# Kernel tuning notes

Hardware: AMD Instinct MI355X
Metric: run time of the kernel (lower is better)

The kernel has to match this reference:

```python
import jax, jax.numpy as jnp
import numpy as np

EXP = 2          # self.exp
NEG = -1e9       # mask fill value
B, N1, DIM, F = 4, 1024, 1024, 4
N = N1 + 1
NTOT = F * N     # 4100


def _normalize(x):
    # L2-normalize along last dim; also return the norm (keepdims)
    n = jnp.sqrt(jnp.sum(x * x, axis=-1, keepdims=True))
    return x / n, n


def setup_inputs() -> dict:
    key = jax.random.key(0)
    k1, k2 = jax.random.split(key)
    lhs = jax.random.normal(k1, (B, N1, DIM), dtype=jnp.float32)
    rhs = jax.random.normal(k2, (B, NTOT, DIM), dtype=jnp.float32)
    return {"lhs": lhs, "rhs": rhs}


def reference(lhs, rhs):
    b, n1, dim = lhs.shape
    n = n1 + 1
    ntot = rhs.shape[1]
    f = ntot // n

    lhs_n, lhs_norm = _normalize(lhs)          # (B,N1,D), (B,N1,1)
    rhs_n, _ = _normalize(rhs)                 # (B,Ntot,D)

    # cosine similarity GEMM + power epilogue
    sim = jnp.einsum('bnd,bmd->bnm', lhs_n, rhs_n) ** EXP   # (B,N1,Ntot)

    # view as (B, N1, F, N); torch masks:
    #   sim4[..., -N1:][~eye] = -1e9   (off-diagonal of last N1 cols)
    #   sim4[..., 0] = -1e9            (first col of each frame)
    # net keep condition: j == i + 1
    sim4 = sim.reshape(b, n1, f, n)
    i = jnp.arange(n1)[:, None, None]   # (N1,1,1)
    j = jnp.arange(n)[None, None, :]    # (1,1,N)
    keep = (j == i + 1)                 # (N1,1,N), broadcasts over F
    sim4 = jnp.where(keep, sim4, jnp.float32(NEG))

    return sim4.reshape(b, n1, ntot), lhs_norm
```

## Files before the change

### kernel.cpp

```cpp
#include <hip/hip_runtime.h>

#define BB   4
#define N1   1024
#define DIM  1024
#define FF   4
#define NN   1025
#define NTOT (FF * NN)
#define SIM_TOTAL ((size_t)BB * N1 * NTOT)
#define NEGV (-1e9f)

__device__ __forceinline__ float wave_reduce_sum(float v) {
#pragma unroll
    for (int off = 32; off > 0; off >>= 1)
        v += __shfl_down(v, off, 64);
    return v;
}

__global__ __launch_bounds__(256)
void lcs_kernel(const float* __restrict__ lhs,
                const float* __restrict__ rhs,
                float* __restrict__ out) {
    const int row = blockIdx.x;
    const int b   = row >> 10;
    const int i   = row & (N1 - 1);
    const int tid = threadIdx.x;

    const float4* lrow = (const float4*)(lhs + (size_t)row * DIM);
    const float4 lv = lrow[tid];
    float p_l2 = lv.x * lv.x + lv.y * lv.y + lv.z * lv.z + lv.w * lv.w;

    float p_dot[FF], p_r2[FF];
#pragma unroll
    for (int f = 0; f < FF; ++f) {
        const size_t rrow_idx = (size_t)b * NTOT + (size_t)f * NN + (i + 1);
        const float4* rrow = (const float4*)(rhs + rrow_idx * DIM);
        const float4 rv = rrow[tid];
        p_dot[f] = lv.x * rv.x + lv.y * rv.y + lv.z * rv.z + lv.w * rv.w;
        p_r2[f]  = rv.x * rv.x + rv.y * rv.y + rv.z * rv.z + rv.w * rv.w;
    }

    float4* orow4 = (float4*)(out + (size_t)row * NTOT);
    const float4 negv = make_float4(NEGV, NEGV, NEGV, NEGV);
#pragma unroll
    for (int k = tid; k < NTOT / 4; k += 256)
        orow4[k] = negv;

    float vals[9];
    vals[0] = p_l2;
#pragma unroll
    for (int f = 0; f < FF; ++f) {
        vals[1 + 2 * f] = p_dot[f];
        vals[2 + 2 * f] = p_r2[f];
    }

    __shared__ float red[4][9];
    const int wave = tid >> 6;
    const int lane = tid & 63;
#pragma unroll
    for (int q = 0; q < 9; ++q) {
        const float r = wave_reduce_sum(vals[q]);
        if (lane == 0) red[wave][q] = r;
    }
    __syncthreads();

    if (tid == 0) {
        float s[9];
#pragma unroll
        for (int q = 0; q < 9; ++q)
            s[q] = red[0][q] + red[1][q] + red[2][q] + red[3][q];

        const float l2 = s[0];
        float* orow = out + (size_t)row * NTOT;
#pragma unroll
        for (int f = 0; f < FF; ++f) {
            const float dot = s[1 + 2 * f];
            const float r2  = s[2 + 2 * f];
            orow[f * NN + i + 1] = (dot * dot) / (l2 * r2);
        }
        out[SIM_TOTAL + row] = sqrtf(l2);
    }
}

extern "C" void kernel_launch(void* const* d_in, const int* in_sizes, int n_in,
                              void* d_out, int out_size, void* d_ws, size_t ws_size,
                              hipStream_t stream) {
    const float* lhs = (const float*)d_in[0];
    const float* rhs = (const float*)d_in[1];
    float* out = (float*)d_out;

    lcs_kernel<<<BB * N1, 256, 0, stream>>>(lhs, rhs, out);
}
```

Before: 126.7 us.

## Split mask fill into separate kernel and use one wave per row for dots

Moves the -1e9 fill of the similarity output into a standalone grid-stride kernel. The dot/norm kernel now assigns one wave per output row and reduces entirely with xor shuffles, removing shared memory and the block barrier. The aim is to decouple the write-bandwidth-bound fill from the latency-bound reductions. It adds a second launch and separate passes over the output.

```diff
diff --git a/kernel.cpp b/kernel.cpp
--- a/kernel.cpp
+++ b/kernel.cpp
@@ -9,75 +9,75 @@
 #define SIM_TOTAL ((size_t)BB * N1 * NTOT)
 #define NEGV (-1e9f)
 
-__device__ __forceinline__ float wave_reduce_sum(float v) {
-#pragma unroll
-    for (int off = 32; off > 0; off >>= 1)
-        v += __shfl_down(v, off, 64);
-    return v;
+__global__ __launch_bounds__(256)
+void fill_kernel(float4* __restrict__ out4, int total4) {
+    const float4 negv = make_float4(NEGV, NEGV, NEGV, NEGV);
+    const int stride = gridDim.x * 256;
+    for (int k = blockIdx.x * 256 + threadIdx.x; k < total4; k += stride)
+        out4[k] = negv;
 }
 
 __global__ __launch_bounds__(256)
-void lcs_kernel(const float* __restrict__ lhs,
+void dot_kernel(const float* __restrict__ lhs,
                 const float* __restrict__ rhs,
                 float* __restrict__ out) {
-    const int row = blockIdx.x;
-    const int b   = row >> 10;
-    const int i   = row & (N1 - 1);
-    const int tid = threadIdx.x;
+    const int row  = blockIdx.x * 4 + (threadIdx.x >> 6);
+    const int lane = threadIdx.x & 63;
+    const int b    = row >> 10;
+    const int i    = row & (N1 - 1);
 
     const float4* lrow = (const float4*)(lhs + (size_t)row * DIM);
-    const float4 lv = lrow[tid];
-    float p_l2 = lv.x * lv.x + lv.y * lv.y + lv.z * lv.z + lv.w * lv.w;
+    float4 lv[4];
+#pragma unroll
+    for (int k = 0; k < 4; ++k)
+        lv[k] = lrow[lane + 64 * k];
 
-    float p_dot[FF], p_r2[FF];
+    float l2 = 0.f;
+#pragma unroll
+    for (int k = 0; k < 4; ++k)
+        l2 += lv[k].x * lv[k].x + lv[k].y * lv[k].y +
+              lv[k].z * lv[k].z + lv[k].w * lv[k].w;
+
+    float dotf[FF], r2f[FF];
 #pragma unroll
     for (int f = 0; f < FF; ++f) {
         const size_t rrow_idx = (size_t)b * NTOT + (size_t)f * NN + (i + 1);
         const float4* rrow = (const float4*)(rhs + rrow_idx * DIM);
-        const float4 rv = rrow[tid];
-        p_dot[f] = lv.x * rv.x + lv.y * rv.y + lv.z * rv.z + lv.w * rv.w;
-        p_r2[f]  = rv.x * rv.x + rv.y * rv.y + rv.z * rv.z + rv.w * rv.w;
+        float d = 0.f, r2 = 0.f;
+#pragma unroll
+        for (int k = 0; k < 4; ++k) {
+            const float4 rv = rrow[lane + 64 * k];
+            d  += lv[k].x * rv.x + lv[k].y * rv.y + lv[k].z * rv.z + lv[k].w * rv.w;
+            r2 += rv.x * rv.x + rv.y * rv.y + rv.z * rv.z + rv.w * rv.w;
+        }
+        dotf[f] = d;
+        r2f[f]  = r2;
     }
 
-    float4* orow4 = (float4*)(out + (size_t)row * NTOT);
-    const float4 negv = make_float4(NEGV, NEGV, NEGV, NEGV);
-#pragma unroll
-    for (int k = tid; k < NTOT / 4; k += 256)
-        orow4[k] = negv;
-
     float vals[9];
-    vals[0] = p_l2;
+    vals[0] = l2;
 #pragma unroll
     for (int f = 0; f < FF; ++f) {
-        vals[1 + 2 * f] = p_dot[f];
-        vals[2 + 2 * f] = p_r2[f];
+        vals[1 + 2 * f] = dotf[f];
+        vals[2 + 2 * f] = r2f[f];
+    }
+#pragma unroll
+    for (int q = 0; q < 9; ++q) {
+#pragma unroll
+        for (int off = 1; off < 64; off <<= 1)
+            vals[q] += __shfl_xor(vals[q], off, 64);
     }
 
-    __shared__ float red[4][9];
-    const int wave = tid >> 6;
-    const int lane = tid & 63;
-#pragma unroll
-    for (int q = 0; q < 9; ++q) {
-        const float r = wave_reduce_sum(vals[q]);
-        if (lane == 0) red[wave][q] = r;
-    }
-    __syncthreads();
-
-    if (tid == 0) {
-        float s[9];
-#pragma unroll
-        for (int q = 0; q < 9; ++q)
-            s[q] = red[0][q] + red[1][q] + red[2][q] + red[3][q];
-
-        const float l2 = s[0];
+    if (lane == 0) {
+        const float L2 = vals[0];
         float* orow = out + (size_t)row * NTOT;
 #pragma unroll
         for (int f = 0; f < FF; ++f) {
-            const float dot = s[1 + 2 * f];
-            const float r2  = s[2 + 2 * f];
-            orow[f * NN + i + 1] = (dot * dot) / (l2 * r2);
+            const float d  = vals[1 + 2 * f];
+            const float r2 = vals[2 + 2 * f];
+            orow[f * NN + i + 1] = (d * d) / (L2 * r2);
         }
-        out[SIM_TOTAL + row] = sqrtf(l2);
+        out[SIM_TOTAL + row] = sqrtf(L2);
     }
 }
 
@@ -88,5 +88,7 @@
     const float* rhs = (const float*)d_in[1];
     float* out = (float*)d_out;
 
-    lcs_kernel<<<BB * N1, 256, 0, stream>>>(lhs, rhs, out);
+    const int total4 = (int)(SIM_TOTAL / 4);
+    fill_kernel<<<2048, 256, 0, stream>>>((float4*)out, total4);
+    dot_kernel<<<(BB * N1) / 4, 256, 0, stream>>>(lhs, rhs, out);
 }
```

New measurement: 134.7 us. 6.4% more time.
